# Kernel tuning notes

Measured on AMD Instinct MI355X. Metric: run time of the kernel, lower is better.

Reference implementation:

```python
import jax, jax.numpy as jnp
import numpy as np

K = 9          # neighbors (module default k=9, dilation=1 -> plain top-k)
COUT = 256     # out_channels
BN_EPS = 1e-5


def setup_inputs() -> dict:
    key = jax.random.key(0)
    k1, k2 = jax.random.split(key, 2)
    x = jax.random.normal(k1, (8, 128, 2048, 1), jnp.float32)          # [B,C,N,1]
    W = jax.random.normal(k2, (COUT, 2 * 128), jnp.float32) * 0.05     # 1x1 conv weight [Cout, 2C]
    gamma = jnp.ones((COUT,), jnp.float32)                             # BN affine scale
    beta = jnp.zeros((COUT,), jnp.float32)                             # BN affine shift
    return {"x": x, "W": W, "gamma": gamma, "beta": beta}


def reference(x, W, gamma, beta):
    # x: [B, C, N, 1] channels-first point features
    xt = jnp.transpose(x[..., 0], (0, 2, 1))                           # [B, N, C]
    B, N, C = xt.shape

    # --- dense KNN graph (matrix form): squared euclidean distance, k nearest ---
    sq = jnp.sum(xt * xt, axis=-1)                                     # [B, N]
    dist = sq[:, :, None] - 2.0 * jnp.einsum('bnc,bmc->bnm', xt, xt) + sq[:, None, :]
    _, nn_idx = jax.lax.top_k(-dist, K)                                # [B, N, K] neighbor indices

    # --- EdgeConv gather: x_i = center, x_j = neighbor ---
    x_j = jax.vmap(lambda f, i: f[i])(xt, nn_idx)                      # [B, N, K, C]
    x_i = xt[:, :, None, :]                                            # [B, N, 1, C]
    feat = jnp.concatenate(
        [jnp.broadcast_to(x_i, (B, N, K, C)), x_j - x_i], axis=-1)     # [B, N, K, 2C]

    # --- 1x1 conv (no bias) as GEMM over channel dim ---
    h = jnp.einsum('bnkc,oc->bnko', feat, W)                           # [B, N, K, Cout]

    # --- BatchNorm2d (training-mode batch stats over B,N,K per channel) ---
    mean = jnp.mean(h, axis=(0, 1, 2))
    var = jnp.var(h, axis=(0, 1, 2))
    hn = (h - mean) * jax.lax.rsqrt(var + BN_EPS) * gamma + beta

    # --- ReLU then max over k neighbors ---
    out = jnp.max(jax.nn.relu(hn), axis=2)                             # [B, N, Cout]
    return jnp.transpose(out, (0, 2, 1))                               # [B, Cout, N]
```

## Files before the change

kernel.cpp:

```cpp
#include <hip/hip_runtime.h>
#include <float.h>
#include <math.h>

#define BATCH 8
#define CHN   128
#define NPTS  2048
#define KNN   9
#define NOUT  256
#define TOTCNT (BATCH*NPTS*KNN)

typedef __attribute__((ext_vector_type(8))) short short8;
typedef __attribute__((ext_vector_type(4))) float f32x4;

__device__ __forceinline__ unsigned short f2bf(float f) {
    unsigned int u = __float_as_uint(f);
    unsigned int r = (u + 0x7FFFu + ((u >> 16) & 1u)) >> 16;
    return (unsigned short)r;
}
__device__ __forceinline__ float bf2f(unsigned short h) {
    return __uint_as_float(((unsigned int)h) << 16);
}

__global__ __launch_bounds__(256) void prep_kernel(const float* __restrict__ x,
                                                   const float* __restrict__ W,
                                                   unsigned short* __restrict__ xhi,
                                                   unsigned short* __restrict__ xlo,
                                                   unsigned short* __restrict__ whi,
                                                   unsigned short* __restrict__ wlo,
                                                   float* __restrict__ sqh) {
    __shared__ float xt[128 * 65];
    __shared__ float psq[256];
    const int b = blockIdx.x, tid = threadIdx.x;
    if (blockIdx.y == 32) {
#pragma unroll
        for (int e = 0; e < 32; ++e) {
            int idx = e * 256 + tid;
            int r = b * 64 + (idx >> 7), c = idx & 127;
            float v = (r < 256) ? (W[r * 256 + c] - W[r * 256 + 128 + c])
                                : W[(r - 256) * 256 + 128 + c];
            unsigned short h = f2bf(v);
            float hf = bf2f(h);
            whi[r * 128 + c] = h;
            wlo[r * 128 + c] = f2bf(v - hf);
        }
        return;
    }
    const int n0 = blockIdx.y * 64;
#pragma unroll 4
    for (int p = 0; p < 32; ++p) {
        int c = p * 4 + (tid >> 6), n = tid & 63;
        xt[c * 65 + n] = x[((size_t)b * CHN + c) * NPTS + n0 + n];
    }
    __syncthreads();
    const int n = tid >> 2, cq = tid & 3;
    size_t row = (size_t)(b * NPTS + n0 + n) * CHN;
    float s = 0.f;
#pragma unroll 8
    for (int j = 0; j < 32; ++j) {
        int c = cq * 32 + j;
        float f = xt[c * 65 + n];
        unsigned short h = f2bf(f);
        float hf = bf2f(h);
        unsigned short l = f2bf(f - hf);
        xhi[row + c] = h;
        xlo[row + c] = l;
        s += f * f;
    }
    psq[tid] = s;
    __syncthreads();
    if (tid < 64)
        sqh[b * NPTS + n0 + tid] =
            0.5f * (psq[tid*4] + psq[tid*4+1] + psq[tid*4+2] + psq[tid*4+3]);
}

__global__ __launch_bounds__(256) void knn_mfma(const unsigned short* __restrict__ xhi,
                                                const unsigned short* __restrict__ xlo,
                                                const float* __restrict__ sqh,
                                                float* __restrict__ pd,
                                                int* __restrict__ pi) {
    __shared__ __align__(16) float dts[64 * 132];

    const int tid = threadIdx.x;
    const int b = blockIdx.x, q0 = blockIdx.y * 64, ms = blockIdx.z;
    const int msbase = ms * 512;
    const int wv = tid >> 6, lane = tid & 63;
    const int quad = lane >> 4, col = lane & 15;
    const int koff = quad * 8;
    const int mcol0 = wv * 32;
    const size_t xb = (size_t)b * NPTS * CHN;

    float dl[KNN]; int il[KNN];
#pragma unroll
    for (int k = 0; k < KNN; ++k) { dl[k] = FLT_MAX; il[k] = 0; }

    const int qsc = tid >> 2, ss = tid & 3;
    const int cb = ss * 32;

    auto ins = [&](float v, int idx) {
        if (v < dl[KNN - 1]) {
            bool c0b = v < dl[0];
#pragma unroll
            for (int k = KNN - 1; k >= 1; --k) {
                bool sh   = v < dl[k - 1];
                bool here = v < dl[k];
                float nd = sh ? dl[k - 1] : (here ? v : dl[k]);
                int   ni = sh ? il[k - 1] : (here ? idx : il[k]);
                dl[k] = nd; il[k] = ni;
            }
            if (c0b) { dl[0] = v; il[0] = idx; }
        }
    };

    for (int iter = 0; iter < 4; ++iter) {
        const int mbase = msbase + iter * 128;
        float sm[2];
#pragma unroll
        for (int j = 0; j < 2; ++j)
            sm[j] = sqh[b * NPTS + mbase + mcol0 + j * 16 + col];

        f32x4 acc[4][2];
#pragma unroll
        for (int i = 0; i < 4; ++i)
#pragma unroll
            for (int j = 0; j < 2; ++j) acc[i][j] = (f32x4)0.f;

        for (int chk = 0; chk < 4; ++chk) {
            short8 ah[4], al[4];
#pragma unroll
            for (int i = 0; i < 4; ++i) {
                size_t g = xb + (size_t)(q0 + i * 16 + col) * CHN + chk * 32 + koff;
                ah[i] = *(const short8*)&xhi[g];
                al[i] = *(const short8*)&xlo[g];
            }
#pragma unroll
            for (int j = 0; j < 2; ++j) {
                size_t g = xb + (size_t)(mbase + mcol0 + j * 16 + col) * CHN + chk * 32 + koff;
                short8 bh = *(const short8*)&xhi[g];
                short8 bl = *(const short8*)&xlo[g];
#pragma unroll
                for (int i = 0; i < 4; ++i) {
                    acc[i][j] = __builtin_amdgcn_mfma_f32_16x16x32_bf16(ah[i], bh, acc[i][j], 0, 0, 0);
                    acc[i][j] = __builtin_amdgcn_mfma_f32_16x16x32_bf16(ah[i], bl, acc[i][j], 0, 0, 0);
                    acc[i][j] = __builtin_amdgcn_mfma_f32_16x16x32_bf16(al[i], bh, acc[i][j], 0, 0, 0);
                }
            }
        }

        __syncthreads();
#pragma unroll
        for (int j = 0; j < 2; ++j)
#pragma unroll
            for (int i = 0; i < 4; ++i)
#pragma unroll
                for (int r = 0; r < 4; ++r) {
                    int q_ = i * 16 + quad * 4 + r;
                    dts[q_ * 132 + mcol0 + j * 16 + col] = sm[j] - acc[i][j][r];
                }
        __syncthreads();
        const int ibase = mbase + cb;
#pragma unroll
        for (int jj = 0; jj < 8; ++jj) {
            float4 v = *(const float4*)&dts[qsc * 132 + cb + jj * 4];
            float mn4 = fminf(fminf(v.x, v.y), fminf(v.z, v.w));
            if (mn4 < dl[KNN - 1]) {
                int ib = ibase + jj * 4;
                ins(v.x, ib); ins(v.y, ib + 1); ins(v.z, ib + 2); ins(v.w, ib + 3);
            }
        }
    }

    __syncthreads();
    float* md = dts;
    int*   mi = (int*)(dts + 2304);
#pragma unroll
    for (int k = 0; k < KNN; ++k) {
        md[qsc * 36 + ss * 9 + k] = dl[k];
        mi[qsc * 36 + ss * 9 + k] = il[k];
    }
    __syncthreads();
    if (tid < 64) {
        int base = tid * 36;
        int p0 = 0, p1 = 0, p2 = 0, p3 = 0;
        size_t ob = ((size_t)(b * NPTS + q0 + tid) * 4 + ms) * KNN;
        for (int k = 0; k < KNN; ++k) {
            float v0 = (p0 < KNN) ? md[base + p0]      : FLT_MAX;
            float v1 = (p1 < KNN) ? md[base + 9 + p1]  : FLT_MAX;
            float v2 = (p2 < KNN) ? md[base + 18 + p2] : FLT_MAX;
            float v3 = (p3 < KNN) ? md[base + 27 + p3] : FLT_MAX;
            float best = v0; int sel = 0;
            if (v1 < best) { best = v1; sel = 1; }
            if (v2 < best) { best = v2; sel = 2; }
            if (v3 < best) { best = v3; sel = 3; }
            int idx;
            if      (sel == 0) { idx = mi[base + p0];      p0++; }
            else if (sel == 1) { idx = mi[base + 9 + p1];  p1++; }
            else if (sel == 2) { idx = mi[base + 18 + p2]; p2++; }
            else               { idx = mi[base + 27 + p3]; p3++; }
            pd[ob + k] = best;
            pi[ob + k] = idx;
        }
    }
}

__global__ __launch_bounds__(256) void pq_mfma(const unsigned short* __restrict__ xhi,
                                               const unsigned short* __restrict__ xlo,
                                               const unsigned short* __restrict__ whi,
                                               const unsigned short* __restrict__ wlo,
                                               float* __restrict__ p,
                                               unsigned short* __restrict__ q) {
    const int tid = threadIdx.x;
    const int b = blockIdx.x, nt = blockIdx.y, ot = blockIdx.z;
    const int wv = tid >> 6, lane = tid & 63;
    const int quad = lane >> 4, col = lane & 15;
    const int koff = quad * 8;
    const size_t xb = (size_t)b * NPTS * CHN;
    const int nbase = nt * 256 + wv * 64;
    const int obase = ot * 64;

    f32x4 acc[4][4];
#pragma unroll
    for (int i = 0; i < 4; ++i)
#pragma unroll
        for (int j = 0; j < 4; ++j) acc[i][j] = (f32x4)0.f;

    for (int chk = 0; chk < 4; ++chk) {
        short8 ah[4], al[4];
#pragma unroll
        for (int i = 0; i < 4; ++i) {
            size_t g = xb + (size_t)(nbase + i * 16 + col) * CHN + chk * 32 + koff;
            ah[i] = *(const short8*)&xhi[g];
            al[i] = *(const short8*)&xlo[g];
        }
#pragma unroll
        for (int j = 0; j < 4; ++j) {
            size_t g = (size_t)(obase + j * 16 + col) * CHN + chk * 32 + koff;
            short8 bh = *(const short8*)&whi[g];
            short8 bl = *(const short8*)&wlo[g];
#pragma unroll
            for (int i = 0; i < 4; ++i) {
                acc[i][j] = __builtin_amdgcn_mfma_f32_16x16x32_bf16(ah[i], bh, acc[i][j], 0, 0, 0);
                acc[i][j] = __builtin_amdgcn_mfma_f32_16x16x32_bf16(ah[i], bl, acc[i][j], 0, 0, 0);
                acc[i][j] = __builtin_amdgcn_mfma_f32_16x16x32_bf16(al[i], bh, acc[i][j], 0, 0, 0);
            }
        }
    }
#pragma unroll
    for (int i = 0; i < 4; ++i)
#pragma unroll
        for (int j = 0; j < 4; ++j) {
            int oc = (obase + j * 16 + col) & 255;
#pragma unroll
            for (int r = 0; r < 4; ++r) {
                int n = nbase + i * 16 + quad * 4 + r;
                size_t off = (size_t)(b * NPTS + n) * NOUT + oc;
                if (ot < 4) p[off] = acc[i][j][r];
                else        q[off] = f2bf(acc[i][j][r]);
            }
        }
}

__global__ __launch_bounds__(256) void stats2_kernel(const float* __restrict__ p,
                                                     const unsigned short* __restrict__ q,
                                                     const float* __restrict__ pd,
                                                     const int* __restrict__ pi,
                                                     float* __restrict__ stats,
                                                     unsigned int* __restrict__ hmm) {
    __shared__ int idx_s[16 * KNN];
    const int b = blockIdx.x, n0 = blockIdx.y * 16;
    const int o = threadIdx.x;
    if (threadIdx.x < 16) {
        size_t g = (size_t)(b * NPTS + n0 + threadIdx.x) * 36;
        const float* d = pd + g;
        const int*   i = pi + g;
        int p0 = 0, p1 = 0, p2 = 0, p3 = 0;
#pragma unroll
        for (int k = 0; k < KNN; ++k) {
            float v0 = (p0 < KNN) ? d[p0]      : FLT_MAX;
            float v1 = (p1 < KNN) ? d[9 + p1]  : FLT_MAX;
            float v2 = (p2 < KNN) ? d[18 + p2] : FLT_MAX;
            float v3 = (p3 < KNN) ? d[27 + p3] : FLT_MAX;
            float best = v0; int sel = 0;
            if (v1 < best) { best = v1; sel = 1; }
            if (v2 < best) { best = v2; sel = 2; }
            if (v3 < best) { best = v3; sel = 3; }
            int idx;
            if      (sel == 0) { idx = i[p0];      p0++; }
            else if (sel == 1) { idx = i[9 + p1];  p1++; }
            else if (sel == 2) { idx = i[18 + p2]; p2++; }
            else               { idx = i[27 + p3]; p3++; }
            idx_s[threadIdx.x * KNN + k] = idx;
        }
    }
    __syncthreads();
    const unsigned short* qb = q + (size_t)b * NPTS * NOUT + o;
    float s = 0.f, ss = 0.f;
    for (int qq = 0; qq < 16; qq += 2) {
        size_t off0 = (size_t)(b * NPTS + n0 + qq) * NOUT + o;
        size_t off1 = off0 + NOUT;
        float pv0 = p[off0], pv1 = p[off1];
        float h0[KNN], h1[KNN];
#pragma unroll
        for (int k = 0; k < KNN; ++k)
            h0[k] = bf2f(qb[(size_t)idx_s[qq * KNN + k] * NOUT]);
#pragma unroll
        for (int k = 0; k < KNN; ++k)
            h1[k] = bf2f(qb[(size_t)idx_s[(qq + 1) * KNN + k] * NOUT]);
        float mx0 = -FLT_MAX, mn0 = FLT_MAX, mx1 = -FLT_MAX, mn1 = FLT_MAX;
#pragma unroll
        for (int k = 0; k < KNN; ++k) {
            float a = pv0 + h0[k], c = pv1 + h1[k];
            s += a + c; ss += a * a + c * c;
            mx0 = fmaxf(mx0, a); mn0 = fminf(mn0, a);
            mx1 = fmaxf(mx1, c); mn1 = fminf(mn1, c);
        }
        hmm[off0] = ((unsigned int)f2bf(mx0) << 16) | f2bf(mn0);
        hmm[off1] = ((unsigned int)f2bf(mx1) << 16) | f2bf(mn1);
    }
    atomicAdd(&stats[b * 512 + o], s);
    atomicAdd(&stats[b * 512 + NOUT + o], ss);
}

__global__ __launch_bounds__(256) void final_kernel(const unsigned int* __restrict__ hmm,
                                                    const float* __restrict__ stats,
                                                    const float* __restrict__ gamma,
                                                    const float* __restrict__ beta,
                                                    float* __restrict__ out) {
    __shared__ float tr[256 * 17];
    const int b = blockIdx.x, n0 = blockIdx.y * 16;
    const int o = threadIdx.x;
    float sum = 0.f, sumsq = 0.f;
#pragma unroll
    for (int i = 0; i < 8; ++i) {
        sum   += stats[i * 512 + o];
        sumsq += stats[i * 512 + NOUT + o];
    }
    const float inv = 1.f / (float)TOTCNT;
    float mean = sum * inv;
    float var  = sumsq * inv - mean * mean;
    float g    = gamma[o] / sqrtf(var + 1e-5f);
    float bet  = beta[o];
    const bool pos = (g >= 0.f);
    for (int qq = 0; qq < 16; ++qq) {
        size_t off = (size_t)(b * NPTS + n0 + qq) * NOUT + o;
        unsigned int w = hmm[off];
        float v = bf2f(pos ? (unsigned short)(w >> 16) : (unsigned short)(w & 0xFFFFu));
        float hn = (v - mean) * g + bet;
        tr[o * 17 + qq] = fmaxf(hn, 0.f);
    }
    __syncthreads();
    int oo = threadIdx.x >> 4, qq = threadIdx.x & 15;
    for (int pass = 0; pass < 16; ++pass) {
        int o_ = pass * 16 + oo;
        out[((size_t)b * NOUT + o_) * NPTS + n0 + qq] = tr[o_ * 17 + qq];
    }
}

extern "C" void kernel_launch(void* const* d_in, const int* in_sizes, int n_in,
                              void* d_out, int out_size, void* d_ws, size_t ws_size,
                              hipStream_t stream) {
    (void)in_sizes; (void)n_in; (void)out_size; (void)ws_size;
    const float* x     = (const float*)d_in[0];
    const float* W     = (const float*)d_in[1];
    const float* gamma = (const float*)d_in[2];
    const float* beta  = (const float*)d_in[3];
    float* out = (float*)d_out;

    char* ws = (char*)d_ws;
    float*          p     = (float*)ws;
    unsigned short* q     = (unsigned short*)(ws + (16u << 20));
    unsigned short* xhi   = (unsigned short*)(ws + (24u << 20));
    unsigned short* xlo   = (unsigned short*)(ws + (28u << 20));
    unsigned int*   hmm   = (unsigned int*)(ws + (32u << 20));
    unsigned short* whi   = (unsigned short*)(ws + (48u << 20));
    unsigned short* wlo   = (unsigned short*)(ws + (48u << 20) + 131072);
    float*          pd    = (float*)(ws + (49u << 20));
    int*            pi    = (int*)  (ws + (52u << 20));
    float*          sqh   = (float*)(ws + (55u << 20));
    float*          stats = (float*)(ws + (55u << 20) + 65536);

    hipMemsetAsync(stats, 0, 8 * 512 * sizeof(float), stream);
    prep_kernel  <<<dim3(8, 33),    256, 0, stream>>>(x, W, xhi, xlo, whi, wlo, sqh);
    knn_mfma     <<<dim3(8, 32, 4), 256, 0, stream>>>(xhi, xlo, sqh, pd, pi);
    pq_mfma      <<<dim3(8, 8, 8),  256, 0, stream>>>(xhi, xlo, whi, wlo, p, q);
    stats2_kernel<<<dim3(8, 128),   256, 0, stream>>>(p, q, pd, pi, stats, hmm);
    final_kernel <<<dim3(8, 128),   256, 0, stream>>>(hmm, stats, gamma, beta, out);
}
```

Baseline: 211.9 us.

## Fuse stats and BN/ReLU output kernels via cooperative grid sync

Merges the statistics/neighbor-max kernel and the final normalization kernel into one cooperative kernel that keeps the packed max/min values in shared memory and uses a grid-wide sync before applying batch-norm. This removes the global hmm write/read round trip and one kernel launch. The stats zeroing also moves into prep_kernel, replacing the memset. The cost is that the 1024-block grid must be fully co-resident for the cooperative launch, which constrains occupancy and adds grid-barrier overhead.

```diff
diff --git a/kernel.cpp b/kernel.cpp
--- a/kernel.cpp
+++ b/kernel.cpp
@@ -1,6 +1,9 @@
 #include <hip/hip_runtime.h>
+#include <hip/hip_cooperative_groups.h>
 #include <float.h>
 #include <math.h>
+
+namespace cg = cooperative_groups;
 
 #define BATCH 8
 #define CHN   128
@@ -27,11 +30,14 @@
                                                    unsigned short* __restrict__ xlo,
                                                    unsigned short* __restrict__ whi,
                                                    unsigned short* __restrict__ wlo,
-                                                   float* __restrict__ sqh) {
+                                                   float* __restrict__ sqh,
+                                                   float* __restrict__ stats) {
     __shared__ float xt[128 * 65];
     __shared__ float psq[256];
     const int b = blockIdx.x, tid = threadIdx.x;
     if (blockIdx.y == 32) {
+        stats[b * 512 + tid] = 0.f;
+        stats[b * 512 + 256 + tid] = 0.f;
 #pragma unroll
         for (int e = 0; e < 32; ++e) {
             int idx = e * 256 + tid;
@@ -259,15 +265,20 @@
         }
 }
 
-__global__ __launch_bounds__(256) void stats2_kernel(const float* __restrict__ p,
-                                                     const unsigned short* __restrict__ q,
-                                                     const float* __restrict__ pd,
-                                                     const int* __restrict__ pi,
-                                                     float* __restrict__ stats,
-                                                     unsigned int* __restrict__ hmm) {
-    __shared__ int idx_s[16 * KNN];
+__global__ __launch_bounds__(256) void fused_tail_kernel(const float* __restrict__ p,
+                                                         const unsigned short* __restrict__ q,
+                                                         const float* __restrict__ pd,
+                                                         const int* __restrict__ pi,
+                                                         float* __restrict__ stats,
+                                                         const float* __restrict__ gamma,
+                                                         const float* __restrict__ beta,
+                                                         float* __restrict__ out) {
+    __shared__ unsigned int hmm_s[16 * 257];
+    __shared__ int   idx_s[16 * KNN];
+    __shared__ float g_s[256], bet_s[256], mean_s[256];
     const int b = blockIdx.x, n0 = blockIdx.y * 16;
     const int o = threadIdx.x;
+
     if (threadIdx.x < 16) {
         size_t g = (size_t)(b * NPTS + n0 + threadIdx.x) * 36;
         const float* d = pd + g;
@@ -292,6 +303,7 @@
         }
     }
     __syncthreads();
+
     const unsigned short* qb = q + (size_t)b * NPTS * NOUT + o;
     float s = 0.f, ss = 0.f;
     for (int qq = 0; qq < 16; qq += 2) {
@@ -313,45 +325,38 @@
             mx0 = fmaxf(mx0, a); mn0 = fminf(mn0, a);
             mx1 = fmaxf(mx1, c); mn1 = fminf(mn1, c);
         }
-        hmm[off0] = ((unsigned int)f2bf(mx0) << 16) | f2bf(mn0);
-        hmm[off1] = ((unsigned int)f2bf(mx1) << 16) | f2bf(mn1);
+        hmm_s[qq * 257 + o]       = ((unsigned int)f2bf(mx0) << 16) | f2bf(mn0);
+        hmm_s[(qq + 1) * 257 + o] = ((unsigned int)f2bf(mx1) << 16) | f2bf(mn1);
     }
     atomicAdd(&stats[b * 512 + o], s);
     atomicAdd(&stats[b * 512 + NOUT + o], ss);
-}
-
-__global__ __launch_bounds__(256) void final_kernel(const unsigned int* __restrict__ hmm,
-                                                    const float* __restrict__ stats,
-                                                    const float* __restrict__ gamma,
-                                                    const float* __restrict__ beta,
-                                                    float* __restrict__ out) {
-    __shared__ float tr[256 * 17];
-    const int b = blockIdx.x, n0 = blockIdx.y * 16;
-    const int o = threadIdx.x;
-    float sum = 0.f, sumsq = 0.f;
-#pragma unroll
-    for (int i = 0; i < 8; ++i) {
-        sum   += stats[i * 512 + o];
-        sumsq += stats[i * 512 + NOUT + o];
-    }
-    const float inv = 1.f / (float)TOTCNT;
-    float mean = sum * inv;
-    float var  = sumsq * inv - mean * mean;
-    float g    = gamma[o] / sqrtf(var + 1e-5f);
-    float bet  = beta[o];
-    const bool pos = (g >= 0.f);
-    for (int qq = 0; qq < 16; ++qq) {
-        size_t off = (size_t)(b * NPTS + n0 + qq) * NOUT + o;
-        unsigned int w = hmm[off];
-        float v = bf2f(pos ? (unsigned short)(w >> 16) : (unsigned short)(w & 0xFFFFu));
-        float hn = (v - mean) * g + bet;
-        tr[o * 17 + qq] = fmaxf(hn, 0.f);
-    }
-    __syncthreads();
-    int oo = threadIdx.x >> 4, qq = threadIdx.x & 15;
+    __threadfence();
+    cg::this_grid().sync();
+
+    {
+        float sum = 0.f, sumsq = 0.f;
+#pragma unroll
+        for (int i = 0; i < 8; ++i) {
+            sum   += stats[i * 512 + o];
+            sumsq += stats[i * 512 + NOUT + o];
+        }
+        const float inv = 1.f / (float)TOTCNT;
+        float mean = sum * inv;
+        float var  = sumsq * inv - mean * mean;
+        g_s[o]    = gamma[o] / sqrtf(var + 1e-5f);
+        bet_s[o]  = beta[o];
+        mean_s[o] = mean;
+    }
+    __syncthreads();
+
+    const int oo = threadIdx.x >> 4, qq2 = threadIdx.x & 15;
     for (int pass = 0; pass < 16; ++pass) {
         int o_ = pass * 16 + oo;
-        out[((size_t)b * NOUT + o_) * NPTS + n0 + qq] = tr[o_ * 17 + qq];
+        float g = g_s[o_];
+        unsigned int w = hmm_s[qq2 * 257 + o_];
+        float v = bf2f((g >= 0.f) ? (unsigned short)(w >> 16) : (unsigned short)(w & 0xFFFFu));
+        float hn = (v - mean_s[o_]) * g + bet_s[o_];
+        out[((size_t)b * NOUT + o_) * NPTS + n0 + qq2] = fmaxf(hn, 0.f);
     }
 }
 
@@ -370,18 +375,19 @@
     unsigned short* q     = (unsigned short*)(ws + (16u << 20));
     unsigned short* xhi   = (unsigned short*)(ws + (24u << 20));
     unsigned short* xlo   = (unsigned short*)(ws + (28u << 20));
-    unsigned int*   hmm   = (unsigned int*)(ws + (32u << 20));
-    unsigned short* whi   = (unsigned short*)(ws + (48u << 20));
-    unsigned short* wlo   = (unsigned short*)(ws + (48u << 20) + 131072);
-    float*          pd    = (float*)(ws + (49u << 20));
-    int*            pi    = (int*)  (ws + (52u << 20));
-    float*          sqh   = (float*)(ws + (55u << 20));
-    float*          stats = (float*)(ws + (55u << 20) + 65536);
-
-    hipMemsetAsync(stats, 0, 8 * 512 * sizeof(float), stream);
-    prep_kernel  <<<dim3(8, 33),    256, 0, stream>>>(x, W, xhi, xlo, whi, wlo, sqh);
-    knn_mfma     <<<dim3(8, 32, 4), 256, 0, stream>>>(xhi, xlo, sqh, pd, pi);
-    pq_mfma      <<<dim3(8, 8, 8),  256, 0, stream>>>(xhi, xlo, whi, wlo, p, q);
-    stats2_kernel<<<dim3(8, 128),   256, 0, stream>>>(p, q, pd, pi, stats, hmm);
-    final_kernel <<<dim3(8, 128),   256, 0, stream>>>(hmm, stats, gamma, beta, out);
-}
+    unsigned short* whi   = (unsigned short*)(ws + (32u << 20));
+    unsigned short* wlo   = (unsigned short*)(ws + (32u << 20) + 131072);
+    float*          pd    = (float*)(ws + (33u << 20));
+    int*            pi    = (int*)  (ws + (36u << 20));
+    float*          sqh   = (float*)(ws + (39u << 20));
+    float*          stats = (float*)(ws + (39u << 20) + 65536);
+
+    prep_kernel<<<dim3(8, 33),    256, 0, stream>>>(x, W, xhi, xlo, whi, wlo, sqh, stats);
+    knn_mfma   <<<dim3(8, 32, 4), 256, 0, stream>>>(xhi, xlo, sqh, pd, pi);
+    pq_mfma    <<<dim3(8, 8, 8),  256, 0, stream>>>(xhi, xlo, whi, wlo, p, q);
+
+    void* fargs[] = { (void*)&p, (void*)&q, (void*)&pd, (void*)&pi,
+                      (void*)&stats, (void*)&gamma, (void*)&beta, (void*)&out };
+    hipLaunchCooperativeKernel((void*)fused_tail_kernel, dim3(8, 128), dim3(256),
+                               fargs, 0, stream);
+}
```

Result: slower. 406.9 us (+92.0%).

## Merge KNN and PQ GEMM into one launch and fold stats zeroing into prep

Applied to the files above, without the earlier changes.

The KNN distance kernel and the W projection GEMM are combined into a single grid: z<4 blocks do KNN and z>=4 blocks compute a smaller 64x32 projection tile each. Because the two independent workloads share one launch, they can run concurrently on the GPU and fill idle CUs. The memset of the BN stats buffer is removed, and the W-prep blocks of prep_kernel now zero it. The smaller projection tile reduces per-block register use and reuse of the W fragments, and it may also change occupancy for the KNN path, since both paths now share one compiled kernel.

```diff
diff --git a/kernel.cpp b/kernel.cpp
--- a/kernel.cpp
+++ b/kernel.cpp
@@ -27,11 +27,14 @@
                                                    unsigned short* __restrict__ xlo,
                                                    unsigned short* __restrict__ whi,
                                                    unsigned short* __restrict__ wlo,
-                                                   float* __restrict__ sqh) {
+                                                   float* __restrict__ sqh,
+                                                   float* __restrict__ stats) {
     __shared__ float xt[128 * 65];
     __shared__ float psq[256];
     const int b = blockIdx.x, tid = threadIdx.x;
     if (blockIdx.y == 32) {
+        stats[b * 512 + tid] = 0.f;
+        stats[b * 512 + 256 + tid] = 0.f;
 #pragma unroll
         for (int e = 0; e < 32; ++e) {
             int idx = e * 256 + tid;
@@ -73,21 +76,77 @@
             0.5f * (psq[tid*4] + psq[tid*4+1] + psq[tid*4+2] + psq[tid*4+3]);
 }
 
-__global__ __launch_bounds__(256) void knn_mfma(const unsigned short* __restrict__ xhi,
-                                                const unsigned short* __restrict__ xlo,
-                                                const float* __restrict__ sqh,
-                                                float* __restrict__ pd,
-                                                int* __restrict__ pi) {
+__global__ __launch_bounds__(256) void knnpq_mfma(const unsigned short* __restrict__ xhi,
+                                                  const unsigned short* __restrict__ xlo,
+                                                  const float* __restrict__ sqh,
+                                                  const unsigned short* __restrict__ whi,
+                                                  const unsigned short* __restrict__ wlo,
+                                                  float* __restrict__ pd,
+                                                  int* __restrict__ pi,
+                                                  float* __restrict__ p,
+                                                  unsigned short* __restrict__ q) {
     __shared__ __align__(16) float dts[64 * 132];
 
     const int tid = threadIdx.x;
-    const int b = blockIdx.x, q0 = blockIdx.y * 64, ms = blockIdx.z;
-    const int msbase = ms * 512;
+    const int b = blockIdx.x;
     const int wv = tid >> 6, lane = tid & 63;
     const int quad = lane >> 4, col = lane & 15;
     const int koff = quad * 8;
+    const size_t xb = (size_t)b * NPTS * CHN;
+
+    if (blockIdx.z >= 4) {
+        const int nt = blockIdx.y >> 2;
+        const int ot = ((blockIdx.y & 3) << 2) | (blockIdx.z - 4);
+        const int nbase = nt * 256 + wv * 64;
+        const int obase = ot * 32;
+
+        f32x4 acc[4][2];
+#pragma unroll
+        for (int i = 0; i < 4; ++i)
+#pragma unroll
+            for (int j = 0; j < 2; ++j) acc[i][j] = (f32x4)0.f;
+
+        for (int chk = 0; chk < 4; ++chk) {
+            short8 ah[4], al[4];
+#pragma unroll
+            for (int i = 0; i < 4; ++i) {
+                size_t g = xb + (size_t)(nbase + i * 16 + col) * CHN + chk * 32 + koff;
+                ah[i] = *(const short8*)&xhi[g];
+                al[i] = *(const short8*)&xlo[g];
+            }
+#pragma unroll
+            for (int j = 0; j < 2; ++j) {
+                size_t g = (size_t)(obase + j * 16 + col) * CHN + chk * 32 + koff;
+                short8 bh = *(const short8*)&whi[g];
+                short8 bl = *(const short8*)&wlo[g];
+#pragma unroll
+                for (int i = 0; i < 4; ++i) {
+                    acc[i][j] = __builtin_amdgcn_mfma_f32_16x16x32_bf16(ah[i], bh, acc[i][j], 0, 0, 0);
+                    acc[i][j] = __builtin_amdgcn_mfma_f32_16x16x32_bf16(ah[i], bl, acc[i][j], 0, 0, 0);
+                    acc[i][j] = __builtin_amdgcn_mfma_f32_16x16x32_bf16(al[i], bh, acc[i][j], 0, 0, 0);
+                }
+            }
+        }
+#pragma unroll
+        for (int i = 0; i < 4; ++i)
+#pragma unroll
+            for (int j = 0; j < 2; ++j) {
+                int brow = obase + j * 16 + col;
+                int oc = brow & 255;
+#pragma unroll
+                for (int r = 0; r < 4; ++r) {
+                    int n = nbase + i * 16 + quad * 4 + r;
+                    size_t off = (size_t)(b * NPTS + n) * NOUT + oc;
+                    if (ot < 8) p[off] = acc[i][j][r];
+                    else        q[off] = f2bf(acc[i][j][r]);
+                }
+            }
+        return;
+    }
+
+    const int q0 = blockIdx.y * 64, ms = blockIdx.z;
+    const int msbase = ms * 512;
     const int mcol0 = wv * 32;
-    const size_t xb = (size_t)b * NPTS * CHN;
 
     float dl[KNN]; int il[KNN];
 #pragma unroll
@@ -202,63 +261,6 @@
     }
 }
 
-__global__ __launch_bounds__(256) void pq_mfma(const unsigned short* __restrict__ xhi,
-                                               const unsigned short* __restrict__ xlo,
-                                               const unsigned short* __restrict__ whi,
-                                               const unsigned short* __restrict__ wlo,
-                                               float* __restrict__ p,
-                                               unsigned short* __restrict__ q) {
-    const int tid = threadIdx.x;
-    const int b = blockIdx.x, nt = blockIdx.y, ot = blockIdx.z;
-    const int wv = tid >> 6, lane = tid & 63;
-    const int quad = lane >> 4, col = lane & 15;
-    const int koff = quad * 8;
-    const size_t xb = (size_t)b * NPTS * CHN;
-    const int nbase = nt * 256 + wv * 64;
-    const int obase = ot * 64;
-
-    f32x4 acc[4][4];
-#pragma unroll
-    for (int i = 0; i < 4; ++i)
-#pragma unroll
-        for (int j = 0; j < 4; ++j) acc[i][j] = (f32x4)0.f;
-
-    for (int chk = 0; chk < 4; ++chk) {
-        short8 ah[4], al[4];
-#pragma unroll
-        for (int i = 0; i < 4; ++i) {
-            size_t g = xb + (size_t)(nbase + i * 16 + col) * CHN + chk * 32 + koff;
-            ah[i] = *(const short8*)&xhi[g];
-            al[i] = *(const short8*)&xlo[g];
-        }
-#pragma unroll
-        for (int j = 0; j < 4; ++j) {
-            size_t g = (size_t)(obase + j * 16 + col) * CHN + chk * 32 + koff;
-            short8 bh = *(const short8*)&whi[g];
-            short8 bl = *(const short8*)&wlo[g];
-#pragma unroll
-            for (int i = 0; i < 4; ++i) {
-                acc[i][j] = __builtin_amdgcn_mfma_f32_16x16x32_bf16(ah[i], bh, acc[i][j], 0, 0, 0);
-                acc[i][j] = __builtin_amdgcn_mfma_f32_16x16x32_bf16(ah[i], bl, acc[i][j], 0, 0, 0);
-                acc[i][j] = __builtin_amdgcn_mfma_f32_16x16x32_bf16(al[i], bh, acc[i][j], 0, 0, 0);
-            }
-        }
-    }
-#pragma unroll
-    for (int i = 0; i < 4; ++i)
-#pragma unroll
-        for (int j = 0; j < 4; ++j) {
-            int oc = (obase + j * 16 + col) & 255;
-#pragma unroll
-            for (int r = 0; r < 4; ++r) {
-                int n = nbase + i * 16 + quad * 4 + r;
-                size_t off = (size_t)(b * NPTS + n) * NOUT + oc;
-                if (ot < 4) p[off] = acc[i][j][r];
-                else        q[off] = f2bf(acc[i][j][r]);
-            }
-        }
-}
-
 __global__ __launch_bounds__(256) void stats2_kernel(const float* __restrict__ p,
                                                      const unsigned short* __restrict__ q,
                                                      const float* __restrict__ pd,
@@ -378,10 +380,8 @@
     float*          sqh   = (float*)(ws + (55u << 20));
     float*          stats = (float*)(ws + (55u << 20) + 65536);
 
-    hipMemsetAsync(stats, 0, 8 * 512 * sizeof(float), stream);
-    prep_kernel  <<<dim3(8, 33),    256, 0, stream>>>(x, W, xhi, xlo, whi, wlo, sqh);
-    knn_mfma     <<<dim3(8, 32, 4), 256, 0, stream>>>(xhi, xlo, sqh, pd, pi);
-    pq_mfma      <<<dim3(8, 8, 8),  256, 0, stream>>>(xhi, xlo, whi, wlo, p, q);
+    prep_kernel  <<<dim3(8, 33),    256, 0, stream>>>(x, W, xhi, xlo, whi, wlo, sqh, stats);
+    knnpq_mfma   <<<dim3(8, 32, 8), 256, 0, stream>>>(xhi, xlo, sqh, whi, wlo, pd, pi, p, q);
     stats2_kernel<<<dim3(8, 128),   256, 0, stream>>>(p, q, pd, pi, stats, hmm);
     final_kernel <<<dim3(8, 128),   256, 0, stream>>>(hmm, stats, gamma, beta, out);
 }
```

Result: no change. 209.5 us (-1.1%).
